# Kernel optimization log

Measured on AMD Instinct MI355X. Metric: run time of the kernel, lower is better.

## Reference

```python
import jax, jax.numpy as jnp
import numpy as np

B, H, L, T, V = 256, 512, 3, 200, 100  # batch, hidden, lstm layers, decode steps (text_max_len-1), vocab


def setup_inputs() -> dict:
    key = jax.random.key(0)
    ks = jax.random.split(key, 12)
    s = 0.04  # ~1/sqrt(512), keeps gates in a sane range like trained weights
    return {
        "feat": jax.random.normal(ks[0], (B, H), jnp.float32),
        "visual_w": jax.random.normal(ks[1], (H, H), jnp.float32) * s,
        "visual_b": jax.random.normal(ks[2], (H,), jnp.float32) * s,
        "embed": jax.random.normal(ks[3], (V, H), jnp.float32),
        "w_ih": jax.random.normal(ks[4], (L, 4 * H, H), jnp.float32) * s,
        "w_hh": jax.random.normal(ks[5], (L, 4 * H, H), jnp.float32) * s,
        "b_ih": jax.random.normal(ks[6], (L, 4 * H), jnp.float32) * s,
        "b_hh": jax.random.normal(ks[7], (L, 4 * H), jnp.float32) * s,
        "proj_w1": jax.random.normal(ks[8], (2 * H, H), jnp.float32) * s,
        "proj_b1": jax.random.normal(ks[9], (2 * H,), jnp.float32) * s,
        "proj_w2": jax.random.normal(ks[10], (V, 2 * H), jnp.float32) * s,
        "proj_b2": jax.random.normal(ks[11], (V,), jnp.float32) * s,
        "start_idx": 1,  # tokenizer.char2idx[sos_token]
    }


def _lstm_stack_step(h, c, x, w_ih, w_hh, b_ih, b_hh):
    # h, c: [L, B, H]; x: [B, H]. PyTorch gate order: i, f, g, o.
    hs, cs = [], []
    for l in range(L):
        gates = x @ w_ih[l].T + b_ih[l] + h[l] @ w_hh[l].T + b_hh[l]  # [B, 4H]
        i, f, g, o = jnp.split(gates, 4, axis=-1)
        c_new = jax.nn.sigmoid(f) * c[l] + jax.nn.sigmoid(i) * jnp.tanh(g)
        h_new = jax.nn.sigmoid(o) * jnp.tanh(c_new)
        hs.append(h_new)
        cs.append(c_new)
        x = h_new  # inter-layer dropout is identity in eval mode
    return jnp.stack(hs), jnp.stack(cs), x


def reference(feat, visual_w, visual_b, embed, w_ih, w_hh, b_ih, b_hh,
              proj_w1, proj_b1, proj_w2, proj_b2, start_idx):
    # encoder feature -> visual_proj (applied once in forward, once more in _init_hidden)
    feat1 = feat @ visual_w.T + visual_b
    h0_layer = feat1 @ visual_w.T + visual_b           # same weights for every layer
    h0 = jnp.broadcast_to(h0_layer, (L, B, H))
    c0 = jnp.zeros((L, B, H), jnp.float32)
    x0 = jnp.broadcast_to(embed[start_idx], (B, H))    # embedded <sos>

    def step(carry, _):
        h, c, x = carry
        h, c, top = _lstm_stack_step(h, c, x, w_ih, w_hh, b_ih, b_hh)
        # next input is the top-layer output, detached (inp = out[-1:].detach())
        return (h, c, jax.lax.stop_gradient(top)), top

    (_, _, _), outs = jax.lax.scan(step, (h0, c0, x0), None, length=T)  # outs: [T, B, H]
    res = outs.transpose(1, 0, 2)                                       # [B, T, H]
    hmid = jax.nn.gelu(res @ proj_w1.T + proj_b1, approximate=False)    # [B, T, 2H]
    logits = hmid @ proj_w2.T + proj_b2                                  # [B, T, V]
    return logits.transpose(0, 2, 1)                                     # [B, V, T]
```

## Files before the change

### kernel.cpp

```cpp
#include <hip/hip_runtime.h>
#include <hip/hip_bf16.h>
#include <hip/hip_fp16.h>

#define NB 256
#define NH 512
#define NL 3
#define NT 200
#define NV 100
#define NVP 112
#define NG 2048
#define NK 1024
#define NS (NT * NL)

using f16x8 = __attribute__((ext_vector_type(8))) _Float16;
using f32x4 = __attribute__((ext_vector_type(4))) float;
using u32x4 = __attribute__((ext_vector_type(4))) unsigned int;

__device__ __forceinline__ float sigf(float x) { return 1.f / (1.f + __expf(-x)); }
__device__ __forceinline__ float tanhf_(float x) { return 2.f / (1.f + __expf(-2.f * x)) - 1.f; }

__global__ void k_probe(int* __restrict__ rowmap, int* __restrict__ colmap) {
  const int lane = threadIdx.x & 63;
  f16x8 a, b;
  const _Float16 idv = (_Float16)(float)(lane & 15);
  const _Float16 inv = (_Float16)(1.f / 32.f);
#pragma unroll
  for (int j = 0; j < 8; ++j) { a[j] = idv; b[j] = inv; }
  f32x4 d = {0.f, 0.f, 0.f, 0.f};
  d = __builtin_amdgcn_mfma_f32_16x16x32_f16(a, b, d, 0, 0, 0);
#pragma unroll
  for (int r = 0; r < 4; ++r) rowmap[lane * 4 + r] = (int)(d[r] + 0.5f);
#pragma unroll
  for (int j = 0; j < 8; ++j) { a[j] = inv; b[j] = idv; }
  f32x4 e = {0.f, 0.f, 0.f, 0.f};
  e = __builtin_amdgcn_mfma_f32_16x16x32_f16(a, b, e, 0, 0, 0);
#pragma unroll
  for (int r = 0; r < 4; ++r) colmap[lane * 4 + r] = (int)(e[r] + 0.5f);
}

__global__ void k_prep_w(const float* __restrict__ w_ih, const float* __restrict__ w_hh,
                         const float* __restrict__ b_ih, const float* __restrict__ b_hh,
                         _Float16* __restrict__ Wih, _Float16* __restrict__ Whh,
                         float* __restrict__ bias) {
  const int stride = gridDim.x * blockDim.x;
  const int tid0 = blockIdx.x * blockDim.x + threadIdx.x;
  for (int idx = tid0; idx < NL * NG * NH; idx += stride) {
    const int k = idx & (NH - 1);
    const int r = (idx >> 9) & (NG - 1);
    const int l = idx >> 20;
    const int hu = r >> 2, g = r & 3;
    const size_t soff = ((size_t)(l * NG + g * NH + hu)) * NH + k;
    Wih[idx] = (_Float16)w_ih[soff];
    Whh[idx] = (_Float16)w_hh[soff];
  }
  for (int idx = tid0; idx < NL * NG; idx += stride) {
    const int r = idx & (NG - 1);
    const int l = idx >> 11;
    const int hu = r >> 2, g = r & 3;
    const int srow = l * NG + g * NH + hu;
    bias[idx] = b_ih[srow] + b_hh[srow];
  }
}

__global__ void k_prep_misc(const float* __restrict__ embed, const int* __restrict__ start_idx,
                            const float* __restrict__ w1, const float* __restrict__ b1,
                            const float* __restrict__ w2, const float* __restrict__ b2,
                            _Float16* __restrict__ x0, _Float16* __restrict__ pw1, float* __restrict__ pb1,
                            _Float16* __restrict__ pw2, float* __restrict__ pb2, int* __restrict__ flags) {
  const int stride = gridDim.x * blockDim.x;
  const int tid0 = blockIdx.x * blockDim.x + threadIdx.x;
  for (int i = tid0; i < 256 * 16; i += stride) flags[i] = 0;
  const int st = start_idx[0];
  for (int i = tid0; i < NB * NH; i += stride)
    x0[i] = (_Float16)embed[(size_t)st * NH + (i & (NH - 1))];
  for (int i = tid0; i < 2 * NH * NH; i += stride)
    pw1[i] = (_Float16)w1[i];
  for (int i = tid0; i < NVP * NK; i += stride) {
    const int r = i >> 10;
    pw2[i] = (_Float16)((r < NV) ? w2[i] : 0.f);
  }
  for (int i = tid0; i < 2 * NH; i += stride) pb1[i] = b1[i];
  for (int i = tid0; i < NVP; i += stride) pb2[i] = (i < NV) ? b2[i] : 0.f;
}

__global__ void k_gemv512(const float* __restrict__ x, const float* __restrict__ w,
                          const float* __restrict__ bias, float* __restrict__ out) {
  const int b = blockIdx.x;
  __shared__ float xs[NH];
  for (int i = threadIdx.x; i < NH; i += 256) xs[i] = x[(size_t)b * NH + i];
  __syncthreads();
  const int wave = threadIdx.x >> 6, lane = threadIdx.x & 63;
  for (int j = wave; j < NH; j += 4) {
    const float* wr = w + (size_t)j * NH;
    float s = 0.f;
#pragma unroll
    for (int i = 0; i < 8; ++i) s += wr[lane + i * 64] * xs[lane + i * 64];
#pragma unroll
    for (int o = 32; o > 0; o >>= 1) s += __shfl_down(s, o);
    if (lane == 0) out[(size_t)b * NH + j] = s + bias[j];
  }
}

__global__ void k_gemv2_h0(const float* __restrict__ feat1, const float* __restrict__ w,
                           const float* __restrict__ bias, _Float16* __restrict__ h0b) {
  const int b = blockIdx.x;
  __shared__ float xs[NH];
  for (int i = threadIdx.x; i < NH; i += 256) xs[i] = feat1[(size_t)b * NH + i];
  __syncthreads();
  const int wave = threadIdx.x >> 6, lane = threadIdx.x & 63;
  for (int j = wave; j < NH; j += 4) {
    const float* wr = w + (size_t)j * NH;
    float s = 0.f;
#pragma unroll
    for (int i = 0; i < 8; ++i) s += wr[lane + i * 64] * xs[lane + i * 64];
#pragma unroll
    for (int o = 32; o > 0; o >>= 1) s += __shfl_down(s, o);
    if (lane == 0) h0b[(size_t)b * NH + j] = (_Float16)(s + bias[j]);
  }
}

__global__ __launch_bounds__(512) void k_lstm(const _Float16* __restrict__ Wih,
                                              const _Float16* __restrict__ Whh,
                                              const float* __restrict__ bias,
                                              _Float16* hx, const _Float16* __restrict__ h0b,
                                              const _Float16* __restrict__ x0,
                                              _Float16* __restrict__ outs,
                                              const int* __restrict__ rowmap, const int* __restrict__ colmap,
                                              int* flags) {
  const int tid = threadIdx.x;
  const int lane = tid & 63;
  const int wave = tid >> 6;
  const int bid = blockIdx.x;
  const int j = bid & 31;
  const int bm = bid >> 5;
  const int bn = (j & 7) * 4 + (j >> 3);
  const int gbase = bm * 32;
  const int grp = wave >> 2;
  const int wn = wave & 3;
  const int lr = lane & 15;
  const int lh = lane >> 4;
  const int nb0 = bn * 64 + wn * 16;
  __shared__ _Float16 Als[32][536];
  __shared__ float gl[32][65];
  __shared__ float pend[3][32][65];
  __shared__ _Float16 hout[32][16];

  int rm[4], cm[4];
#pragma unroll
  for (int r = 0; r < 4; ++r) {
    rm[r] = rowmap[lane * 4 + r];
    cm[r] = colmap[lane * 4 + r];
  }
  const int bl_ = tid >> 4;
  const int hu = tid & 15;
  float creg[NL] = {0.f, 0.f, 0.f};
  float bsv[NL][4];
#pragma unroll
  for (int l = 0; l < NL; ++l)
#pragma unroll
    for (int g = 0; g < 4; ++g) bsv[l][g] = bias[l * NG + (bn * 16 + hu) * 4 + g];

#define STAGE_A(SRCBASE)                                              \
  do {                                                                \
    const _Float16* _sb = (SRCBASE);                                  \
    _Pragma("unroll") for (int c = 0; c < 4; ++c) {                   \
      const int i_ = tid + c * 512;                                   \
      const int r_ = i_ >> 6;                                         \
      const int cc_ = i_ & 63;                                        \
      u32x4 v_ = *(const volatile u32x4*)(_sb + (size_t)r_ * NH + cc_ * 8); \
      *(u32x4*)&Als[r_][cc_ * 8] = v_;                                \
    }                                                                 \
  } while (0)

  STAGE_A(h0b + (size_t)(bm * 32) * NH);
  __syncthreads();
  if (grp == 0) {
#pragma unroll 1
    for (int lp = 0; lp < 3; ++lp) {
      const _Float16* bp = Whh + ((size_t)(lp * NG + nb0 + lr)) * NH + lh * 8;
      f32x4 a0 = {0.f, 0.f, 0.f, 0.f}, a1 = {0.f, 0.f, 0.f, 0.f};
#pragma unroll 4
      for (int kk = 0; kk < 16; ++kk) {
        f16x8 av0 = *(const f16x8*)&Als[lr][kk * 32 + lh * 8];
        f16x8 av1 = *(const f16x8*)&Als[16 + lr][kk * 32 + lh * 8];
        f16x8 bv = *(const f16x8*)(bp + (size_t)kk * 32);
        a0 = __builtin_amdgcn_mfma_f32_16x16x32_f16(av0, bv, a0, 0, 0, 0);
        a1 = __builtin_amdgcn_mfma_f32_16x16x32_f16(av1, bv, a1, 0, 0, 0);
      }
#pragma unroll
      for (int r = 0; r < 4; ++r) {
        pend[lp][rm[r]][wn * 16 + cm[r]] = a0[r];
        pend[lp][16 + rm[r]][wn * 16 + cm[r]] = a1[r];
      }
    }
  }
  __syncthreads();
  STAGE_A(x0 + (size_t)(bm * 32) * NH);
  __syncthreads();

#pragma unroll 1
  for (int t = 0; t < NT; ++t) {
#pragma unroll
    for (int l = 0; l < NL; ++l) {
      const int s = t * 3 + l;
      if (grp == 0) {
        const _Float16* bp = Wih + ((size_t)(l * NG + nb0 + lr)) * NH + lh * 8;
        f32x4 a0 = {0.f, 0.f, 0.f, 0.f}, a1 = {0.f, 0.f, 0.f, 0.f};
#pragma unroll 4
        for (int kk = 0; kk < 16; ++kk) {
          f16x8 av0 = *(const f16x8*)&Als[lr][kk * 32 + lh * 8];
          f16x8 av1 = *(const f16x8*)&Als[16 + lr][kk * 32 + lh * 8];
          f16x8 bv = *(const f16x8*)(bp + (size_t)kk * 32);
          a0 = __builtin_amdgcn_mfma_f32_16x16x32_f16(av0, bv, a0, 0, 0, 0);
          a1 = __builtin_amdgcn_mfma_f32_16x16x32_f16(av1, bv, a1, 0, 0, 0);
        }
#pragma unroll
        for (int r = 0; r < 4; ++r) {
          gl[rm[r]][wn * 16 + cm[r]] = a0[r];
          gl[16 + rm[r]][wn * 16 + cm[r]] = a1[r];
        }
      } else if (s >= 1 && s <= NS - 3) {
        const int l2 = (l == 0) ? 2 : l - 1;
        const _Float16* bp = Whh + ((size_t)(l2 * NG + nb0 + lr)) * NH + lh * 8;
        f32x4 a0 = {0.f, 0.f, 0.f, 0.f}, a1 = {0.f, 0.f, 0.f, 0.f};
#pragma unroll 4
        for (int kk = 0; kk < 16; ++kk) {
          f16x8 av0 = *(const f16x8*)&Als[lr][kk * 32 + lh * 8];
          f16x8 av1 = *(const f16x8*)&Als[16 + lr][kk * 32 + lh * 8];
          f16x8 bv = *(const f16x8*)(bp + (size_t)kk * 32);
          a0 = __builtin_amdgcn_mfma_f32_16x16x32_f16(av0, bv, a0, 0, 0, 0);
          a1 = __builtin_amdgcn_mfma_f32_16x16x32_f16(av1, bv, a1, 0, 0, 0);
        }
#pragma unroll
        for (int r = 0; r < 4; ++r) {
          pend[l2][rm[r]][wn * 16 + cm[r]] = a0[r];
          pend[l2][16 + rm[r]][wn * 16 + cm[r]] = a1[r];
        }
      }
      __syncthreads();
      {
        const float gi = gl[bl_][hu * 4 + 0] + pend[l][bl_][hu * 4 + 0] + bsv[l][0];
        const float gf = gl[bl_][hu * 4 + 1] + pend[l][bl_][hu * 4 + 1] + bsv[l][1];
        const float gg = gl[bl_][hu * 4 + 2] + pend[l][bl_][hu * 4 + 2] + bsv[l][2];
        const float go = gl[bl_][hu * 4 + 3] + pend[l][bl_][hu * 4 + 3] + bsv[l][3];
        const float cn = sigf(gf) * creg[l] + sigf(gi) * tanhf_(gg);
        const float hn = sigf(go) * tanhf_(cn);
        creg[l] = cn;
        hout[bl_][hu] = (_Float16)hn;
      }
      __syncthreads();
      if (wave == 0) {
        const int row = lane >> 1, half = lane & 1;
        _Float16* dst = hx + (size_t)(s & 1) * NB * NH + (size_t)(bm * 32 + row) * NH + bn * 16 + half * 8;
        u32x4 v = *(const u32x4*)&hout[row][half * 8];
        *(volatile u32x4*)dst = v;
        asm volatile("s_waitcnt vmcnt(0)" ::: "memory");
        if (lane == 0) *(volatile int*)&flags[(gbase + j) * 16] = s + 1;
      }
      if (wave == 1 && l == 2) {
        const int row = lane >> 1, half = lane & 1;
        _Float16* dst = outs + ((size_t)t * NB + bm * 32 + row) * NH + bn * 16 + half * 8;
        *(u32x4*)dst = *(const u32x4*)&hout[row][half * 8];
      }
      if (s < NS - 1) {
        if (tid < 32) {
          const volatile int* fp = (const volatile int*)&flags[(gbase + tid) * 16];
          while (*fp < s + 1) __builtin_amdgcn_s_sleep(1);
        }
        __syncthreads();
        STAGE_A(hx + (size_t)(s & 1) * NB * NH + (size_t)(bm * 32) * NH);
        __syncthreads();
      }
    }
  }
#undef STAGE_A
}

__global__ __launch_bounds__(256) void k_proj(const _Float16* __restrict__ outs, const _Float16* __restrict__ pw1,
                                              const float* __restrict__ pb1, const _Float16* __restrict__ pw2,
                                              const float* __restrict__ pb2,
                                              const int* __restrict__ rowmap, const int* __restrict__ colmap,
                                              float* __restrict__ out) {
  const int tid = threadIdx.x;
  const int lane = tid & 63;
  const int wave = tid >> 6;
  const int lr = lane & 15;
  const int lh = lane >> 4;
  const int mbase = blockIdx.x * 16;
  __shared__ _Float16 hm[16][NK + 8];
  int rm[4], cm[4];
#pragma unroll
  for (int r = 0; r < 4; ++r) {
    rm[r] = rowmap[lane * 4 + r];
    cm[r] = colmap[lane * 4 + r];
  }
  const int mrow = mbase + lr;
  const _Float16* ap = outs + ((size_t)(mrow % NT) * NB + (mrow / NT)) * NH + lh * 8;
  for (int nf = 0; nf < 16; ++nf) {
    const int n0 = wave * 256 + nf * 16;
    f32x4 acc = {0.f, 0.f, 0.f, 0.f};
    const _Float16* bp = pw1 + (size_t)(n0 + lr) * NH + lh * 8;
#pragma unroll 4
    for (int kk = 0; kk < 16; ++kk) {
      f16x8 a = *(const f16x8*)(ap + kk * 32);
      f16x8 b = *(const f16x8*)(bp + kk * 32);
      acc = __builtin_amdgcn_mfma_f32_16x16x32_f16(a, b, acc, 0, 0, 0);
    }
#pragma unroll
    for (int r = 0; r < 4; ++r) {
      const float v = acc[r] + pb1[n0 + cm[r]];
      const float gv = 0.5f * v * (1.f + erff(v * 0.70710678118654752f));
      hm[rm[r]][n0 + cm[r]] = (_Float16)gv;
    }
  }
  __syncthreads();
  for (int nf = wave; nf < 7; nf += 4) {
    const int n0 = nf * 16;
    f32x4 acc = {0.f, 0.f, 0.f, 0.f};
    const _Float16* bp = pw2 + (size_t)(n0 + lr) * NK + lh * 8;
#pragma unroll 4
    for (int kk = 0; kk < 32; ++kk) {
      f16x8 a = *(const f16x8*)(&hm[lr][kk * 32 + lh * 8]);
      f16x8 b = *(const f16x8*)(bp + kk * 32);
      acc = __builtin_amdgcn_mfma_f32_16x16x32_f16(a, b, acc, 0, 0, 0);
    }
#pragma unroll
    for (int r = 0; r < 4; ++r) {
      const int v = n0 + cm[r];
      if (v < NV) {
        const int m = mbase + rm[r];
        out[((size_t)(m / NT) * NV + v) * NT + (m % NT)] = acc[r] + pb2[v];
      }
    }
  }
}

extern "C" void kernel_launch(void* const* d_in, const int* in_sizes, int n_in,
                              void* d_out, int out_size, void* d_ws, size_t ws_size,
                              hipStream_t stream) {
  const float* feat = (const float*)d_in[0];
  const float* visual_w = (const float*)d_in[1];
  const float* visual_b = (const float*)d_in[2];
  const float* embed = (const float*)d_in[3];
  const float* w_ih = (const float*)d_in[4];
  const float* w_hh = (const float*)d_in[5];
  const float* b_ih = (const float*)d_in[6];
  const float* b_hh = (const float*)d_in[7];
  const float* proj_w1 = (const float*)d_in[8];
  const float* proj_b1 = (const float*)d_in[9];
  const float* proj_w2 = (const float*)d_in[10];
  const float* proj_b2 = (const float*)d_in[11];
  const int* start_idx = (const int*)d_in[12];
  float* out = (float*)d_out;

  char* ws = (char*)d_ws;
  size_t off = 0;
  auto alloc = [&](size_t bytes) -> void* {
    void* p = ws + off;
    off += (bytes + 255) & ~(size_t)255;
    return p;
  };
  _Float16* Wih = (_Float16*)alloc((size_t)NL * NG * NH * 2);
  _Float16* Whh = (_Float16*)alloc((size_t)NL * NG * NH * 2);
  float* bias = (float*)alloc((size_t)NL * NG * 4);
  _Float16* hx = (_Float16*)alloc((size_t)2 * NB * NH * 2);
  _Float16* h0b = (_Float16*)alloc((size_t)NB * NH * 2);
  _Float16* x0 = (_Float16*)alloc((size_t)NB * NH * 2);
  _Float16* outsb = (_Float16*)alloc((size_t)NT * NB * NH * 2);
  float* feat1 = (float*)alloc((size_t)NB * NH * 4);
  _Float16* pw1 = (_Float16*)alloc((size_t)2 * NH * NH * 2);
  _Float16* pw2 = (_Float16*)alloc((size_t)NVP * NK * 2);
  float* pb1 = (float*)alloc((size_t)2 * NH * 4);
  float* pb2 = (float*)alloc((size_t)NVP * 4);
  int* flags = (int*)alloc(256 * 16 * 4);
  int* rowmap = (int*)alloc(256 * 4);
  int* colmap = (int*)alloc(256 * 4);
  if (off > ws_size) return;

  k_probe<<<dim3(1), dim3(64), 0, stream>>>(rowmap, colmap);
  k_prep_w<<<dim3(2048), dim3(256), 0, stream>>>(w_ih, w_hh, b_ih, b_hh, Wih, Whh, bias);
  k_prep_misc<<<dim3(1024), dim3(256), 0, stream>>>(embed, start_idx, proj_w1, proj_b1, proj_w2, proj_b2,
                                                    x0, pw1, pb1, pw2, pb2, flags);
  k_gemv512<<<dim3(NB), dim3(256), 0, stream>>>(feat, visual_w, visual_b, feat1);
  k_gemv2_h0<<<dim3(NB), dim3(256), 0, stream>>>(feat1, visual_w, visual_b, h0b);
  k_lstm<<<dim3(256), dim3(512), 0, stream>>>(Wih, Whh, bias, hx, h0b, x0, outsb, rowmap, colmap, flags);
  k_proj<<<dim3(3200), dim3(256), 0, stream>>>(outsb, pw1, pb1, pw2, pb2, rowmap, colmap, out);
}
```

Baseline: 4.887 ms.

## Replace flag-based LSTM step barrier with tagged data publish and register weight prefetch

Each thread now publishes its hidden value packed with a step tag into a double-buffered exchange array. Consumers poll that data directly until all tags match, then unpack it into LDS. This removes the separate flag write, the s_waitcnt and flag spin, and the extra LDS staging and barrier on every step. The next layer's weights are also prefetched into registers before the wait, so the weight loads overlap with synchronization. The cost is larger exchange payloads (32 bits per fp16 value), heavier polling traffic, and higher register pressure. The exchange buffer is never zeroed, so correctness relies on leftover workspace contents never carrying a tag equal to the awaited step.

```diff
diff --git a/kernel.cpp b/kernel.cpp
--- a/kernel.cpp
+++ b/kernel.cpp
@@ -66,10 +66,9 @@
                             const float* __restrict__ w1, const float* __restrict__ b1,
                             const float* __restrict__ w2, const float* __restrict__ b2,
                             _Float16* __restrict__ x0, _Float16* __restrict__ pw1, float* __restrict__ pb1,
-                            _Float16* __restrict__ pw2, float* __restrict__ pb2, int* __restrict__ flags) {
+                            _Float16* __restrict__ pw2, float* __restrict__ pb2) {
   const int stride = gridDim.x * blockDim.x;
   const int tid0 = blockIdx.x * blockDim.x + threadIdx.x;
-  for (int i = tid0; i < 256 * 16; i += stride) flags[i] = 0;
   const int st = start_idx[0];
   for (int i = tid0; i < NB * NH; i += stride)
     x0[i] = (_Float16)embed[(size_t)st * NH + (i & (NH - 1))];
@@ -119,22 +118,22 @@
   }
 }
 
-__global__ __launch_bounds__(512) void k_lstm(const _Float16* __restrict__ Wih,
-                                              const _Float16* __restrict__ Whh,
-                                              const float* __restrict__ bias,
-                                              _Float16* hx, const _Float16* __restrict__ h0b,
-                                              const _Float16* __restrict__ x0,
-                                              _Float16* __restrict__ outs,
-                                              const int* __restrict__ rowmap, const int* __restrict__ colmap,
-                                              int* flags) {
+__global__ __launch_bounds__(512, 2) void k_lstm(const _Float16* __restrict__ Wih,
+                                                 const _Float16* __restrict__ Whh,
+                                                 const float* __restrict__ bias,
+                                                 unsigned int* trans,
+                                                 const _Float16* __restrict__ h0b,
+                                                 const _Float16* __restrict__ x0,
+                                                 _Float16* __restrict__ outs,
+                                                 const int* __restrict__ rowmap,
+                                                 const int* __restrict__ colmap) {
   const int tid = threadIdx.x;
   const int lane = tid & 63;
   const int wave = tid >> 6;
   const int bid = blockIdx.x;
-  const int j = bid & 31;
+  const int jj = bid & 31;
   const int bm = bid >> 5;
-  const int bn = (j & 7) * 4 + (j >> 3);
-  const int gbase = bm * 32;
+  const int bn = (jj & 7) * 4 + (jj >> 3);
   const int grp = wave >> 2;
   const int wn = wave & 3;
   const int lr = lane & 15;
@@ -143,7 +142,6 @@
   __shared__ _Float16 Als[32][536];
   __shared__ float gl[32][65];
   __shared__ float pend[3][32][65];
-  __shared__ _Float16 hout[32][16];
 
   int rm[4], cm[4];
 #pragma unroll
@@ -153,6 +151,8 @@
   }
   const int bl_ = tid >> 4;
   const int hu = tid & 15;
+  const int g_ = tid & 15;
+  const int r_ = tid >> 4;
   float creg[NL] = {0.f, 0.f, 0.f};
   float bsv[NL][4];
 #pragma unroll
@@ -160,19 +160,43 @@
 #pragma unroll
     for (int g = 0; g < 4; ++g) bsv[l][g] = bias[l * NG + (bn * 16 + hu) * 4 + g];
 
-#define STAGE_A(SRCBASE)                                              \
-  do {                                                                \
-    const _Float16* _sb = (SRCBASE);                                  \
-    _Pragma("unroll") for (int c = 0; c < 4; ++c) {                   \
-      const int i_ = tid + c * 512;                                   \
-      const int r_ = i_ >> 6;                                         \
-      const int cc_ = i_ & 63;                                        \
-      u32x4 v_ = *(const volatile u32x4*)(_sb + (size_t)r_ * NH + cc_ * 8); \
-      *(u32x4*)&Als[r_][cc_ * 8] = v_;                                \
-    }                                                                 \
+  f16x8 wreg[16];
+
+#define PREFETCH(LX, LZ)                                                          \
+  do {                                                                            \
+    const _Float16* wb = (grp == 0)                                               \
+        ? (Wih + ((size_t)((LX) * NG + nb0 + lr)) * NH + lh * 8)                  \
+        : (Whh + ((size_t)((LZ) * NG + nb0 + lr)) * NH + lh * 8);                 \
+    _Pragma("unroll") for (int k_ = 0; k_ < 16; ++k_)                             \
+        wreg[k_] = *(const f16x8*)(wb + k_ * 32);                                 \
   } while (0)
 
-  STAGE_A(h0b + (size_t)(bm * 32) * NH);
+#define GEMM_TO(DST)                                                              \
+  do {                                                                            \
+    f32x4 a0_ = {0.f, 0.f, 0.f, 0.f}, a1_ = {0.f, 0.f, 0.f, 0.f};                 \
+    _Pragma("unroll") for (int kk = 0; kk < 16; ++kk) {                           \
+      f16x8 av0 = *(const f16x8*)&Als[lr][kk * 32 + lh * 8];                      \
+      f16x8 av1 = *(const f16x8*)&Als[16 + lr][kk * 32 + lh * 8];                 \
+      a0_ = __builtin_amdgcn_mfma_f32_16x16x32_f16(av0, wreg[kk], a0_, 0, 0, 0);  \
+      a1_ = __builtin_amdgcn_mfma_f32_16x16x32_f16(av1, wreg[kk], a1_, 0, 0, 0);  \
+    }                                                                             \
+    _Pragma("unroll") for (int r = 0; r < 4; ++r) {                               \
+      (DST)[rm[r]][wn * 16 + cm[r]] = a0_[r];                                     \
+      (DST)[16 + rm[r]][wn * 16 + cm[r]] = a1_[r];                                \
+    }                                                                             \
+  } while (0)
+
+#define STAGE_PLAIN(SRC)                                                          \
+  do {                                                                            \
+    _Pragma("unroll") for (int c = 0; c < 4; ++c) {                               \
+      const int i_ = tid + c * 512;                                               \
+      const int rr = i_ >> 6, cc = i_ & 63;                                       \
+      *(u32x4*)&Als[rr][cc * 8] =                                                 \
+          *(const u32x4*)((SRC) + (size_t)(bm * 32 + rr) * NH + cc * 8);          \
+    }                                                                             \
+  } while (0)
+
+  STAGE_PLAIN(h0b);
   __syncthreads();
   if (grp == 0) {
 #pragma unroll 1
@@ -194,8 +218,9 @@
       }
     }
   }
-  __syncthreads();
-  STAGE_A(x0 + (size_t)(bm * 32) * NH);
+  PREFETCH(0, 2);
+  __syncthreads();
+  STAGE_PLAIN(x0);
   __syncthreads();
 
 #pragma unroll 1
@@ -204,38 +229,9 @@
     for (int l = 0; l < NL; ++l) {
       const int s = t * 3 + l;
       if (grp == 0) {
-        const _Float16* bp = Wih + ((size_t)(l * NG + nb0 + lr)) * NH + lh * 8;
-        f32x4 a0 = {0.f, 0.f, 0.f, 0.f}, a1 = {0.f, 0.f, 0.f, 0.f};
-#pragma unroll 4
-        for (int kk = 0; kk < 16; ++kk) {
-          f16x8 av0 = *(const f16x8*)&Als[lr][kk * 32 + lh * 8];
-          f16x8 av1 = *(const f16x8*)&Als[16 + lr][kk * 32 + lh * 8];
-          f16x8 bv = *(const f16x8*)(bp + (size_t)kk * 32);
-          a0 = __builtin_amdgcn_mfma_f32_16x16x32_f16(av0, bv, a0, 0, 0, 0);
-          a1 = __builtin_amdgcn_mfma_f32_16x16x32_f16(av1, bv, a1, 0, 0, 0);
-        }
-#pragma unroll
-        for (int r = 0; r < 4; ++r) {
-          gl[rm[r]][wn * 16 + cm[r]] = a0[r];
-          gl[16 + rm[r]][wn * 16 + cm[r]] = a1[r];
-        }
+        GEMM_TO(gl);
       } else if (s >= 1 && s <= NS - 3) {
-        const int l2 = (l == 0) ? 2 : l - 1;
-        const _Float16* bp = Whh + ((size_t)(l2 * NG + nb0 + lr)) * NH + lh * 8;
-        f32x4 a0 = {0.f, 0.f, 0.f, 0.f}, a1 = {0.f, 0.f, 0.f, 0.f};
-#pragma unroll 4
-        for (int kk = 0; kk < 16; ++kk) {
-          f16x8 av0 = *(const f16x8*)&Als[lr][kk * 32 + lh * 8];
-          f16x8 av1 = *(const f16x8*)&Als[16 + lr][kk * 32 + lh * 8];
-          f16x8 bv = *(const f16x8*)(bp + (size_t)kk * 32);
-          a0 = __builtin_amdgcn_mfma_f32_16x16x32_f16(av0, bv, a0, 0, 0, 0);
-          a1 = __builtin_amdgcn_mfma_f32_16x16x32_f16(av1, bv, a1, 0, 0, 0);
-        }
-#pragma unroll
-        for (int r = 0; r < 4; ++r) {
-          pend[l2][rm[r]][wn * 16 + cm[r]] = a0[r];
-          pend[l2][16 + rm[r]][wn * 16 + cm[r]] = a1[r];
-        }
+        GEMM_TO(pend[(l + 2) % 3]);
       }
       __syncthreads();
       {
@@ -246,34 +242,64 @@
         const float cn = sigf(gf) * creg[l] + sigf(gi) * tanhf_(gg);
         const float hn = sigf(go) * tanhf_(cn);
         creg[l] = cn;
-        hout[bl_][hu] = (_Float16)hn;
-      }
-      __syncthreads();
-      if (wave == 0) {
-        const int row = lane >> 1, half = lane & 1;
-        _Float16* dst = hx + (size_t)(s & 1) * NB * NH + (size_t)(bm * 32 + row) * NH + bn * 16 + half * 8;
-        u32x4 v = *(const u32x4*)&hout[row][half * 8];
-        *(volatile u32x4*)dst = v;
-        asm volatile("s_waitcnt vmcnt(0)" ::: "memory");
-        if (lane == 0) *(volatile int*)&flags[(gbase + j) * 16] = s + 1;
-      }
-      if (wave == 1 && l == 2) {
-        const int row = lane >> 1, half = lane & 1;
-        _Float16* dst = outs + ((size_t)t * NB + bm * 32 + row) * NH + bn * 16 + half * 8;
-        *(u32x4*)dst = *(const u32x4*)&hout[row][half * 8];
+        union { _Float16 f; unsigned short u; } hc;
+        hc.f = (_Float16)hn;
+        volatile unsigned int* pub =
+            trans + ((((size_t)bm * 2 + (s & 1)) * 32 + bn) * 32 + bl_) * 16 + hu;
+        *pub = ((unsigned)(s + 1) << 16) | (unsigned)hc.u;
+        if (l == 2) outs[((size_t)t * NB + bm * 32 + bl_) * NH + bn * 16 + hu] = hc.f;
       }
       if (s < NS - 1) {
-        if (tid < 32) {
-          const volatile int* fp = (const volatile int*)&flags[(gbase + tid) * 16];
-          while (*fp < s + 1) __builtin_amdgcn_s_sleep(1);
-        }
+        PREFETCH((l + 1) % 3, l);
+        const unsigned want = (unsigned)(s + 1);
+        const unsigned int* base0 =
+            trans + ((((size_t)bm * 2 + (s & 1)) * 32 + 2 * g_) * 32 + r_) * 16;
+        const unsigned int* base1 = base0 + 512;
+        u32x4 va0, va1, va2, va3, vb0, vb1, vb2, vb3;
+        unsigned msk = 0xffu;
+#define TAGOK(V) (((V)[0] >> 16) == want && ((V)[1] >> 16) == want && \
+                  ((V)[2] >> 16) == want && ((V)[3] >> 16) == want)
+        do {
+          if (msk & 0x01u) va0 = *(const volatile u32x4*)(base0 + 0);
+          if (msk & 0x02u) va1 = *(const volatile u32x4*)(base0 + 4);
+          if (msk & 0x04u) va2 = *(const volatile u32x4*)(base0 + 8);
+          if (msk & 0x08u) va3 = *(const volatile u32x4*)(base0 + 12);
+          if (msk & 0x10u) vb0 = *(const volatile u32x4*)(base1 + 0);
+          if (msk & 0x20u) vb1 = *(const volatile u32x4*)(base1 + 4);
+          if (msk & 0x40u) vb2 = *(const volatile u32x4*)(base1 + 8);
+          if (msk & 0x80u) vb3 = *(const volatile u32x4*)(base1 + 12);
+          if ((msk & 0x01u) && TAGOK(va0)) msk &= ~0x01u;
+          if ((msk & 0x02u) && TAGOK(va1)) msk &= ~0x02u;
+          if ((msk & 0x04u) && TAGOK(va2)) msk &= ~0x04u;
+          if ((msk & 0x08u) && TAGOK(va3)) msk &= ~0x08u;
+          if ((msk & 0x10u) && TAGOK(vb0)) msk &= ~0x10u;
+          if ((msk & 0x20u) && TAGOK(vb1)) msk &= ~0x20u;
+          if ((msk & 0x40u) && TAGOK(vb2)) msk &= ~0x40u;
+          if ((msk & 0x80u) && TAGOK(vb3)) msk &= ~0x80u;
+        } while (msk);
+#undef TAGOK
+#define PK(X, Y) (((X) & 0xffffu) | ((Y) << 16))
+        u32x4 w;
+        w[0] = PK(va0[0], va0[1]); w[1] = PK(va0[2], va0[3]);
+        w[2] = PK(va1[0], va1[1]); w[3] = PK(va1[2], va1[3]);
+        *(u32x4*)&Als[r_][(2 * g_) * 16] = w;
+        w[0] = PK(va2[0], va2[1]); w[1] = PK(va2[2], va2[3]);
+        w[2] = PK(va3[0], va3[1]); w[3] = PK(va3[2], va3[3]);
+        *(u32x4*)&Als[r_][(2 * g_) * 16 + 8] = w;
+        w[0] = PK(vb0[0], vb0[1]); w[1] = PK(vb0[2], vb0[3]);
+        w[2] = PK(vb1[0], vb1[1]); w[3] = PK(vb1[2], vb1[3]);
+        *(u32x4*)&Als[r_][(2 * g_ + 1) * 16] = w;
+        w[0] = PK(vb2[0], vb2[1]); w[1] = PK(vb2[2], vb2[3]);
+        w[2] = PK(vb3[0], vb3[1]); w[3] = PK(vb3[2], vb3[3]);
+        *(u32x4*)&Als[r_][(2 * g_ + 1) * 16 + 8] = w;
+#undef PK
         __syncthreads();
-        STAGE_A(hx + (size_t)(s & 1) * NB * NH + (size_t)(bm * 32) * NH);
-        __syncthreads();
-      }
-    }
-  }
-#undef STAGE_A
+      }
+    }
+  }
+#undef STAGE_PLAIN
+#undef GEMM_TO
+#undef PREFETCH
 }
 
 __global__ __launch_bounds__(256) void k_proj(const _Float16* __restrict__ outs, const _Float16* __restrict__ pw1,
@@ -363,7 +389,7 @@
   _Float16* Wih = (_Float16*)alloc((size_t)NL * NG * NH * 2);
   _Float16* Whh = (_Float16*)alloc((size_t)NL * NG * NH * 2);
   float* bias = (float*)alloc((size_t)NL * NG * 4);
-  _Float16* hx = (_Float16*)alloc((size_t)2 * NB * NH * 2);
+  unsigned int* trans = (unsigned int*)alloc((size_t)8 * 2 * 32 * 32 * 16 * 4);
   _Float16* h0b = (_Float16*)alloc((size_t)NB * NH * 2);
   _Float16* x0 = (_Float16*)alloc((size_t)NB * NH * 2);
   _Float16* outsb = (_Float16*)alloc((size_t)NT * NB * NH * 2);
@@ -372,7 +398,6 @@
   _Float16* pw2 = (_Float16*)alloc((size_t)NVP * NK * 2);
   float* pb1 = (float*)alloc((size_t)2 * NH * 4);
   float* pb2 = (float*)alloc((size_t)NVP * 4);
-  int* flags = (int*)alloc(256 * 16 * 4);
   int* rowmap = (int*)alloc(256 * 4);
   int* colmap = (int*)alloc(256 * 4);
   if (off > ws_size) return;
@@ -380,9 +405,9 @@
   k_probe<<<dim3(1), dim3(64), 0, stream>>>(rowmap, colmap);
   k_prep_w<<<dim3(2048), dim3(256), 0, stream>>>(w_ih, w_hh, b_ih, b_hh, Wih, Whh, bias);
   k_prep_misc<<<dim3(1024), dim3(256), 0, stream>>>(embed, start_idx, proj_w1, proj_b1, proj_w2, proj_b2,
-                                                    x0, pw1, pb1, pw2, pb2, flags);
+                                                    x0, pw1, pb1, pw2, pb2);
   k_gemv512<<<dim3(NB), dim3(256), 0, stream>>>(feat, visual_w, visual_b, feat1);
   k_gemv2_h0<<<dim3(NB), dim3(256), 0, stream>>>(feat1, visual_w, visual_b, h0b);
-  k_lstm<<<dim3(256), dim3(512), 0, stream>>>(Wih, Whh, bias, hx, h0b, x0, outsb, rowmap, colmap, flags);
+  k_lstm<<<dim3(256), dim3(512), 0, stream>>>(Wih, Whh, bias, trans, h0b, x0, outsb, rowmap, colmap);
   k_proj<<<dim3(3200), dim3(256), 0, stream>>>(outsb, pw1, pb1, pw2, pb2, rowmap, colmap, out);
 }
```

Result: slower. 5.709 ms (+16.8%).

## Prefetch LSTM weights into registers, swizzle LDS, and merge flag-wait barriers

Applied to the files above, without the earlier changes.

Each wave now loads its next-step weight slice (16 f16x8 vectors) into registers before the barrier, so the global weight fetch overlaps the gate nonlinearity and the inter-block flag wait instead of sitting on the critical path of the recurrent GEMM. The A tile in LDS drops its padding in favour of an XOR swizzle. Every wave now spins on the 32 producer flags, which lets the hx staging happen right after the spin and removes one __syncthreads per step. It also adds vectorized f32x4 gate reads with the gate buffers padded to 68, and sets launch_bounds(512,2); the extra weight registers raise register pressure and more threads now poll the flags.

```diff
diff --git a/kernel.cpp b/kernel.cpp
--- a/kernel.cpp
+++ b/kernel.cpp
@@ -119,30 +119,31 @@
   }
 }
 
-__global__ __launch_bounds__(512) void k_lstm(const _Float16* __restrict__ Wih,
-                                              const _Float16* __restrict__ Whh,
-                                              const float* __restrict__ bias,
-                                              _Float16* hx, const _Float16* __restrict__ h0b,
-                                              const _Float16* __restrict__ x0,
-                                              _Float16* __restrict__ outs,
-                                              const int* __restrict__ rowmap, const int* __restrict__ colmap,
-                                              int* flags) {
+__global__ __launch_bounds__(512, 2) void k_lstm(const _Float16* __restrict__ Wih,
+                                                 const _Float16* __restrict__ Whh,
+                                                 const float* __restrict__ bias,
+                                                 _Float16* hx, const _Float16* __restrict__ h0b,
+                                                 const _Float16* __restrict__ x0,
+                                                 _Float16* __restrict__ outs,
+                                                 const int* __restrict__ rowmap,
+                                                 const int* __restrict__ colmap,
+                                                 int* flags) {
   const int tid = threadIdx.x;
   const int lane = tid & 63;
   const int wave = tid >> 6;
   const int bid = blockIdx.x;
-  const int j = bid & 31;
+  const int jj = bid & 31;
   const int bm = bid >> 5;
-  const int bn = (j & 7) * 4 + (j >> 3);
+  const int bn = (jj & 7) * 4 + (jj >> 3);
   const int gbase = bm * 32;
   const int grp = wave >> 2;
   const int wn = wave & 3;
   const int lr = lane & 15;
   const int lh = lane >> 4;
   const int nb0 = bn * 64 + wn * 16;
-  __shared__ _Float16 Als[32][536];
-  __shared__ float gl[32][65];
-  __shared__ float pend[3][32][65];
+  __shared__ _Float16 Als[32][512];
+  __shared__ float gl[32][68];
+  __shared__ float pend[3][32][68];
   __shared__ _Float16 hout[32][16];
 
   int rm[4], cm[4];
@@ -160,19 +161,46 @@
 #pragma unroll
     for (int g = 0; g < 4; ++g) bsv[l][g] = bias[l * NG + (bn * 16 + hu) * 4 + g];
 
-#define STAGE_A(SRCBASE)                                              \
-  do {                                                                \
-    const _Float16* _sb = (SRCBASE);                                  \
-    _Pragma("unroll") for (int c = 0; c < 4; ++c) {                   \
-      const int i_ = tid + c * 512;                                   \
-      const int r_ = i_ >> 6;                                         \
-      const int cc_ = i_ & 63;                                        \
-      u32x4 v_ = *(const volatile u32x4*)(_sb + (size_t)r_ * NH + cc_ * 8); \
-      *(u32x4*)&Als[r_][cc_ * 8] = v_;                                \
-    }                                                                 \
+  f16x8 wreg[16];
+
+#define PREFETCH(LX, LZ)                                                          \
+  do {                                                                            \
+    const _Float16* wb = (grp == 0)                                               \
+        ? (Wih + ((size_t)((LX) * NG + nb0 + lr)) * NH + lh * 8)                  \
+        : (Whh + ((size_t)((LZ) * NG + nb0 + lr)) * NH + lh * 8);                 \
+    _Pragma("unroll") for (int k_ = 0; k_ < 16; ++k_)                             \
+        wreg[k_] = *(const f16x8*)(wb + k_ * 32);                                 \
   } while (0)
 
-  STAGE_A(h0b + (size_t)(bm * 32) * NH);
+#define AREAD0(KK) (*(const f16x8*)&Als[lr][(((KK) * 4 + lh) ^ (lr & 7)) * 8])
+#define AREAD1(KK) (*(const f16x8*)&Als[16 + lr][(((KK) * 4 + lh) ^ (lr & 7)) * 8])
+
+#define GEMM_TO(DST)                                                              \
+  do {                                                                            \
+    f32x4 a0_ = {0.f, 0.f, 0.f, 0.f}, a1_ = {0.f, 0.f, 0.f, 0.f};                 \
+    _Pragma("unroll") for (int kk = 0; kk < 16; ++kk) {                           \
+      f16x8 av0 = AREAD0(kk);                                                     \
+      f16x8 av1 = AREAD1(kk);                                                     \
+      a0_ = __builtin_amdgcn_mfma_f32_16x16x32_f16(av0, wreg[kk], a0_, 0, 0, 0);  \
+      a1_ = __builtin_amdgcn_mfma_f32_16x16x32_f16(av1, wreg[kk], a1_, 0, 0, 0);  \
+    }                                                                             \
+    _Pragma("unroll") for (int r = 0; r < 4; ++r) {                               \
+      (DST)[rm[r]][wn * 16 + cm[r]] = a0_[r];                                     \
+      (DST)[16 + rm[r]][wn * 16 + cm[r]] = a1_[r];                                \
+    }                                                                             \
+  } while (0)
+
+#define STAGE_A(SRC, VOLQ)                                                        \
+  do {                                                                            \
+    _Pragma("unroll") for (int c = 0; c < 4; ++c) {                               \
+      const int i_ = tid + c * 512;                                               \
+      const int rr = i_ >> 6, cc = i_ & 63;                                       \
+      u32x4 v_ = *(const VOLQ u32x4*)((SRC) + (size_t)(bm * 32 + rr) * NH + cc * 8); \
+      *(u32x4*)&Als[rr][(cc ^ (rr & 7)) * 8] = v_;                                \
+    }                                                                             \
+  } while (0)
+
+  STAGE_A(h0b, );
   __syncthreads();
   if (grp == 0) {
 #pragma unroll 1
@@ -181,8 +209,8 @@
       f32x4 a0 = {0.f, 0.f, 0.f, 0.f}, a1 = {0.f, 0.f, 0.f, 0.f};
 #pragma unroll 4
       for (int kk = 0; kk < 16; ++kk) {
-        f16x8 av0 = *(const f16x8*)&Als[lr][kk * 32 + lh * 8];
-        f16x8 av1 = *(const f16x8*)&Als[16 + lr][kk * 32 + lh * 8];
+        f16x8 av0 = AREAD0(kk);
+        f16x8 av1 = AREAD1(kk);
         f16x8 bv = *(const f16x8*)(bp + (size_t)kk * 32);
         a0 = __builtin_amdgcn_mfma_f32_16x16x32_f16(av0, bv, a0, 0, 0, 0);
         a1 = __builtin_amdgcn_mfma_f32_16x16x32_f16(av1, bv, a1, 0, 0, 0);
@@ -194,8 +222,9 @@
       }
     }
   }
-  __syncthreads();
-  STAGE_A(x0 + (size_t)(bm * 32) * NH);
+  PREFETCH(0, 2);
+  __syncthreads();
+  STAGE_A(x0, );
   __syncthreads();
 
 #pragma unroll 1
@@ -204,45 +233,19 @@
     for (int l = 0; l < NL; ++l) {
       const int s = t * 3 + l;
       if (grp == 0) {
-        const _Float16* bp = Wih + ((size_t)(l * NG + nb0 + lr)) * NH + lh * 8;
-        f32x4 a0 = {0.f, 0.f, 0.f, 0.f}, a1 = {0.f, 0.f, 0.f, 0.f};
-#pragma unroll 4
-        for (int kk = 0; kk < 16; ++kk) {
-          f16x8 av0 = *(const f16x8*)&Als[lr][kk * 32 + lh * 8];
-          f16x8 av1 = *(const f16x8*)&Als[16 + lr][kk * 32 + lh * 8];
-          f16x8 bv = *(const f16x8*)(bp + (size_t)kk * 32);
-          a0 = __builtin_amdgcn_mfma_f32_16x16x32_f16(av0, bv, a0, 0, 0, 0);
-          a1 = __builtin_amdgcn_mfma_f32_16x16x32_f16(av1, bv, a1, 0, 0, 0);
-        }
-#pragma unroll
-        for (int r = 0; r < 4; ++r) {
-          gl[rm[r]][wn * 16 + cm[r]] = a0[r];
-          gl[16 + rm[r]][wn * 16 + cm[r]] = a1[r];
-        }
+        GEMM_TO(gl);
       } else if (s >= 1 && s <= NS - 3) {
-        const int l2 = (l == 0) ? 2 : l - 1;
-        const _Float16* bp = Whh + ((size_t)(l2 * NG + nb0 + lr)) * NH + lh * 8;
-        f32x4 a0 = {0.f, 0.f, 0.f, 0.f}, a1 = {0.f, 0.f, 0.f, 0.f};
-#pragma unroll 4
-        for (int kk = 0; kk < 16; ++kk) {
-          f16x8 av0 = *(const f16x8*)&Als[lr][kk * 32 + lh * 8];
-          f16x8 av1 = *(const f16x8*)&Als[16 + lr][kk * 32 + lh * 8];
-          f16x8 bv = *(const f16x8*)(bp + (size_t)kk * 32);
-          a0 = __builtin_amdgcn_mfma_f32_16x16x32_f16(av0, bv, a0, 0, 0, 0);
-          a1 = __builtin_amdgcn_mfma_f32_16x16x32_f16(av1, bv, a1, 0, 0, 0);
-        }
-#pragma unroll
-        for (int r = 0; r < 4; ++r) {
-          pend[l2][rm[r]][wn * 16 + cm[r]] = a0[r];
-          pend[l2][16 + rm[r]][wn * 16 + cm[r]] = a1[r];
-        }
-      }
+        GEMM_TO(pend[(l + 2) % 3]);
+      }
+      PREFETCH((l + 1) % 3, l);
       __syncthreads();
       {
-        const float gi = gl[bl_][hu * 4 + 0] + pend[l][bl_][hu * 4 + 0] + bsv[l][0];
-        const float gf = gl[bl_][hu * 4 + 1] + pend[l][bl_][hu * 4 + 1] + bsv[l][1];
-        const float gg = gl[bl_][hu * 4 + 2] + pend[l][bl_][hu * 4 + 2] + bsv[l][2];
-        const float go = gl[bl_][hu * 4 + 3] + pend[l][bl_][hu * 4 + 3] + bsv[l][3];
+        const f32x4 gx = *(const f32x4*)&gl[bl_][hu * 4];
+        const f32x4 gh = *(const f32x4*)&pend[l][bl_][hu * 4];
+        const float gi = gx[0] + gh[0] + bsv[l][0];
+        const float gf = gx[1] + gh[1] + bsv[l][1];
+        const float gg = gx[2] + gh[2] + bsv[l][2];
+        const float go = gx[3] + gh[3] + bsv[l][3];
         const float cn = sigf(gf) * creg[l] + sigf(gi) * tanhf_(gg);
         const float hn = sigf(go) * tanhf_(cn);
         creg[l] = cn;
@@ -255,7 +258,7 @@
         u32x4 v = *(const u32x4*)&hout[row][half * 8];
         *(volatile u32x4*)dst = v;
         asm volatile("s_waitcnt vmcnt(0)" ::: "memory");
-        if (lane == 0) *(volatile int*)&flags[(gbase + j) * 16] = s + 1;
+        if (lane == 0) *(volatile int*)&flags[(gbase + jj) * 16] = s + 1;
       }
       if (wave == 1 && l == 2) {
         const int row = lane >> 1, half = lane & 1;
@@ -263,17 +266,20 @@
         *(u32x4*)dst = *(const u32x4*)&hout[row][half * 8];
       }
       if (s < NS - 1) {
-        if (tid < 32) {
-          const volatile int* fp = (const volatile int*)&flags[(gbase + tid) * 16];
+        if (lane < 32) {
+          const volatile int* fp = (const volatile int*)&flags[(gbase + lane) * 16];
           while (*fp < s + 1) __builtin_amdgcn_s_sleep(1);
         }
+        STAGE_A(hx + (size_t)(s & 1) * NB * NH, volatile);
         __syncthreads();
-        STAGE_A(hx + (size_t)(s & 1) * NB * NH + (size_t)(bm * 32) * NH);
-        __syncthreads();
       }
     }
   }
 #undef STAGE_A
+#undef GEMM_TO
+#undef AREAD0
+#undef AREAD1
+#undef PREFETCH
 }
 
 __global__ __launch_bounds__(256) void k_proj(const _Float16* __restrict__ outs, const _Float16* __restrict__ pw1,
```

After: 5.090 ms. 1.04x slower.
